# Performance work log

Measured on AMD Instinct MI355X. Metric: run time of the kernel, lower is better.

## Reference

```python
import jax, jax.numpy as jnp
import numpy as np

S, B, D, H = 1024, 64, 512, 512


def setup_inputs() -> dict:
    key = jax.random.key(0)
    ks = jax.random.split(key, 9)
    scale_g = 1.0 / np.sqrt(D + H)  # torch Linear default init range
    def lin(k):
        kw, kb = jax.random.split(k)
        W = jax.random.uniform(kw, (H, D + H), jnp.float32, -scale_g, scale_g)
        b = jax.random.uniform(kb, (H,), jnp.float32, -scale_g, scale_g)
        return W, b
    Wf, bf = lin(ks[0])
    Wi, bi = lin(ks[1])
    Wg, bg = lin(ks[2])
    Wo, bo = lin(ks[3])
    inputs = jax.random.normal(ks[4], (S, B, D), jnp.float32)
    return {"inputs": inputs, "Wf": Wf, "bf": bf, "Wi": Wi, "bi": bi,
            "Wg": Wg, "bg": bg, "Wo": Wo, "bo": bo}


def _lstm(inputs, Wf, bf, Wi, bi, Wg, bg, Wo, bo):
    # inputs: (S, B, D). Precompute the input-to-gate GEMMs for all timesteps
    # in one large matmul (same math: Linear(cat([x,h])) = x@Wx.T + h@Wh.T + b).
    Dd = inputs.shape[-1]
    Wx = jnp.concatenate([Wf[:, :Dd], Wi[:, :Dd], Wg[:, :Dd], Wo[:, :Dd]], axis=0)  # (4H, D)
    Wh = jnp.concatenate([Wf[:, Dd:], Wi[:, Dd:], Wg[:, Dd:], Wo[:, Dd:]], axis=0)  # (4H, H)
    b = jnp.concatenate([bf, bi, bg, bo], axis=0)  # (4H,)
    gx = jnp.einsum('sbd,gd->sbg', inputs, Wx) + b  # (S, B, 4H)
    Hh = Wf.shape[0]

    def step(carry, gx_t):
        hx, cx = carry
        gates = gx_t + hx @ Wh.T  # (B, 4H)
        f = jax.nn.sigmoid(gates[:, 0 * Hh:1 * Hh])
        i = jax.nn.sigmoid(gates[:, 1 * Hh:2 * Hh])
        g = jnp.tanh(gates[:, 2 * Hh:3 * Hh])
        o = jax.nn.sigmoid(gates[:, 3 * Hh:4 * Hh])
        cx = f * cx + i * g
        hx = o * jnp.tanh(cx)
        return (hx, cx), hx

    B_ = inputs.shape[1]
    h0 = jnp.zeros((B_, Hh), inputs.dtype)
    c0 = jnp.zeros((B_, Hh), inputs.dtype)
    (hx, cx), outputs = jax.lax.scan(step, (h0, c0), gx)
    return outputs, hx, cx


def reference(inputs, Wf, bf, Wi, bi, Wg, bg, Wo, bo):
    outputs, hx, cx = _lstm(inputs, Wf, bf, Wi, bi, Wg, bg, Wo, bo)
    return outputs, (hx, cx)
```

## Files before the change

### kernel.cpp

```cpp
#include <hip/hip_runtime.h>

typedef __attribute__((ext_vector_type(8))) short short8;
typedef __attribute__((ext_vector_type(4))) float f32x4;
typedef unsigned int u32;
typedef unsigned short u16;

#define SS 1024
#define BB 64
#define DD 512
#define HH 512

#define WS_XB    0x00000000ULL
#define WS_WPX   0x04000000ULL
#define WS_WPH   0x04200000ULL
#define WS_BIAS  0x04400000ULL
#define WS_HB0   0x04402000ULL
#define WS_HB1   0x04422000ULL
#define WS_BAR   0x04442000ULL

__device__ __forceinline__ u16 f2bf(float x) {
  union { float f; u32 u; } v; v.f = x;
  u32 r = v.u + 0x7fffu + ((v.u >> 16) & 1u);
  return (u16)(r >> 16);
}

__device__ __forceinline__ float sigm(float x) {
  return 1.f / (1.f + __expf(-x));
}
__device__ __forceinline__ float tanh_fast(float x) {
  const float e = __expf(-2.f * __builtin_fabsf(x));
  return __builtin_copysignf((1.f - e) / (1.f + e), x);
}

__global__ __launch_bounds__(256) void pack_x(const float* __restrict__ X,
                                              u16* __restrict__ Xb) {
  const size_t i = ((size_t)blockIdx.x * 256 + threadIdx.x) * 4;
  const float4 v = *(const float4*)(X + i);
  uint2 o;
  o.x = (u32)f2bf(v.x) | ((u32)f2bf(v.y) << 16);
  o.y = (u32)f2bf(v.z) | ((u32)f2bf(v.w) << 16);
  *(uint2*)(Xb + i) = o;
}

__global__ __launch_bounds__(128) void pack_w(
    const float* __restrict__ Wf, const float* __restrict__ bf_,
    const float* __restrict__ Wi, const float* __restrict__ bi_,
    const float* __restrict__ Wg, const float* __restrict__ bg_,
    const float* __restrict__ Wo, const float* __restrict__ bo_,
    u16* __restrict__ Wpx, u16* __restrict__ Wph, float* __restrict__ bias) {
  const int c = blockIdx.x;
  const int g = c & 3, u = c >> 2;
  const float* Wsrc = (g == 0 ? Wf : g == 1 ? Wi : g == 2 ? Wg : Wo) + (size_t)u * 1024;
  const int k = threadIdx.x * 4;
  const float4 vx = *(const float4*)(Wsrc + k);
  const float4 vh = *(const float4*)(Wsrc + 512 + k);
  uint2 ox, oh;
  ox.x = (u32)f2bf(vx.x) | ((u32)f2bf(vx.y) << 16);
  ox.y = (u32)f2bf(vx.z) | ((u32)f2bf(vx.w) << 16);
  oh.x = (u32)f2bf(vh.x) | ((u32)f2bf(vh.y) << 16);
  oh.y = (u32)f2bf(vh.z) | ((u32)f2bf(vh.w) << 16);
  *(uint2*)(Wpx + (size_t)c * 512 + k) = ox;
  *(uint2*)(Wph + (size_t)c * 512 + k) = oh;
  if (threadIdx.x == 0)
    bias[c] = (g == 0 ? bf_ : g == 1 ? bi_ : g == 2 ? bg_ : bo_)[u];
}

__global__ __launch_bounds__(256, 1) void lstm_scan(
    const u16* __restrict__ Wph, const u16* __restrict__ Wpx,
    const u16* __restrict__ Xb, const float* __restrict__ bias,
    u16* __restrict__ hb0, u16* __restrict__ hb1,
    float* __restrict__ out, u32* __restrict__ bar) {
  const int w = blockIdx.x;
  const int tid = threadIdx.x;
  const int lane = tid & 63;
  const int wave = tid >> 6;
  const int m0 = w * 16;
  const int kq = (lane >> 4) * 8;
  const int arow = m0 + (lane & 15);
  const int brow = wave * 16 + (lane & 15);
  const int u_loc = lane >> 4;

  short8 ah[16], ax[16];
#pragma unroll
  for (int kf = 0; kf < 16; ++kf) {
    ah[kf] = *(const short8*)(Wph + (size_t)arow * 512 + kf * 32 + kq);
    ax[kf] = *(const short8*)(Wpx + (size_t)arow * 512 + kf * 32 + kq);
  }
  const float4 b4 = *(const float4*)(bias + m0 + u_loc * 4);
  const f32x4 bias_acc = (f32x4){b4.x, b4.y, b4.z, b4.w};

  short8 bx[16];
#pragma unroll
  for (int kf = 0; kf < 16; ++kf)
    bx[kf] = *(const short8*)(Xb + (size_t)brow * 512 + kf * 32 + kq);
  f32x4 x0 = bias_acc, x1 = (f32x4){0.f, 0.f, 0.f, 0.f}, x2 = x1, x3 = x1;
#pragma unroll
  for (int kf = 0; kf < 16; kf += 4) {
    x0 = __builtin_amdgcn_mfma_f32_16x16x32_bf16(ax[kf + 0], bx[kf + 0], x0, 0, 0, 0);
    x1 = __builtin_amdgcn_mfma_f32_16x16x32_bf16(ax[kf + 1], bx[kf + 1], x1, 0, 0, 0);
    x2 = __builtin_amdgcn_mfma_f32_16x16x32_bf16(ax[kf + 2], bx[kf + 2], x2, 0, 0, 0);
    x3 = __builtin_amdgcn_mfma_f32_16x16x32_bf16(ax[kf + 3], bx[kf + 3], x3, 0, 0, 0);
  }
  f32x4 gxcur = (x0 + x1) + (x2 + x3);
#pragma unroll
  for (int kf = 0; kf < 16; ++kf)
    bx[kf] = *(const short8*)(Xb + ((size_t)64 + brow) * 512 + kf * 32 + kq);

  float c_reg = 0.f;
  __shared__ float ho_lds[64][4];
  __shared__ float co_lds[64][4];

#pragma unroll 1
  for (int t = 0; t < SS; ++t) {
    const u16* hcur = (t & 1) ? hb1 : hb0;
    u16* hnxt = (t & 1) ? hb0 : hb1;

    short8 bh[16];
#pragma unroll
    for (int kf = 0; kf < 16; ++kf)
      bh[kf] = *(const short8*)(hcur + (size_t)brow * 512 + kf * 32 + kq);

    f32x4 ac0 = gxcur;
    f32x4 ac1 = (f32x4){0.f, 0.f, 0.f, 0.f}, ac2 = ac1, ac3 = ac1;
#pragma unroll
    for (int kf = 0; kf < 16; kf += 4) {
      ac0 = __builtin_amdgcn_mfma_f32_16x16x32_bf16(ah[kf + 0], bh[kf + 0], ac0, 0, 0, 0);
      ac1 = __builtin_amdgcn_mfma_f32_16x16x32_bf16(ah[kf + 1], bh[kf + 1], ac1, 0, 0, 0);
      ac2 = __builtin_amdgcn_mfma_f32_16x16x32_bf16(ah[kf + 2], bh[kf + 2], ac2, 0, 0, 0);
      ac3 = __builtin_amdgcn_mfma_f32_16x16x32_bf16(ah[kf + 3], bh[kf + 3], ac3, 0, 0, 0);
    }
    const f32x4 accs = (ac0 + ac1) + (ac2 + ac3);

    const float fs = sigm(accs[0]);
    const float is = sigm(accs[1]);
    const float gv = tanh_fast(accs[2]);
    const float os = sigm(accs[3]);
    c_reg = fs * c_reg + is * gv;
    const float hv = os * tanh_fast(c_reg);

    ho_lds[brow][u_loc] = hv;
    co_lds[brow][u_loc] = c_reg;
    __syncthreads();

    if (tid < 64) {
      const float4 h4 = *(const float4*)(ho_lds[tid]);
      uint2 hb;
      hb.x = (u32)f2bf(h4.x) | ((u32)f2bf(h4.y) << 16);
      hb.y = (u32)f2bf(h4.z) | ((u32)f2bf(h4.w) << 16);
      *(uint2*)(hnxt + (size_t)tid * 512 + w * 4) = hb;
    } else if (tid < 128) {
      const int b = tid - 64;
      const float4 h4 = *(const float4*)(ho_lds[b]);
      *(float4*)(out + (size_t)t * 32768 + (size_t)b * 512 + w * 4) = h4;
      if (t == SS - 1) {
        *(float4*)(out + 33554432 + (size_t)b * 512 + w * 4) = h4;
        const float4 c4 = *(const float4*)(co_lds[b]);
        *(float4*)(out + 33554432 + 32768 + (size_t)b * 512 + w * 4) = c4;
      }
    }

    if (t != SS - 1) {
      if (tid == 0)
        __hip_atomic_fetch_add(bar + (blockIdx.x & 7) * 16, 1u,
                               __ATOMIC_RELEASE, __HIP_MEMORY_SCOPE_AGENT);
      __builtin_amdgcn_sched_barrier(0);

      x0 = bias_acc; x1 = (f32x4){0.f, 0.f, 0.f, 0.f}; x2 = x1; x3 = x1;
#pragma unroll
      for (int kf = 0; kf < 16; kf += 4) {
        x0 = __builtin_amdgcn_mfma_f32_16x16x32_bf16(ax[kf + 0], bx[kf + 0], x0, 0, 0, 0);
        x1 = __builtin_amdgcn_mfma_f32_16x16x32_bf16(ax[kf + 1], bx[kf + 1], x1, 0, 0, 0);
        x2 = __builtin_amdgcn_mfma_f32_16x16x32_bf16(ax[kf + 2], bx[kf + 2], x2, 0, 0, 0);
        x3 = __builtin_amdgcn_mfma_f32_16x16x32_bf16(ax[kf + 3], bx[kf + 3], x3, 0, 0, 0);
      }
      gxcur = (x0 + x1) + (x2 + x3);
      const size_t tnx = (size_t)((t + 2 < SS) ? t + 2 : SS - 1) * 64 + brow;
#pragma unroll
      for (int kf = 0; kf < 16; ++kf)
        bx[kf] = *(const short8*)(Xb + tnx * 512 + kf * 32 + kq);

      const u32 target = (u32)(t + 1) * 16u;
      if (tid < 8) {
        int guard = 0;
#pragma unroll 1
        while (__hip_atomic_load(bar + tid * 16, __ATOMIC_RELAXED,
                                 __HIP_MEMORY_SCOPE_AGENT) < target &&
               ++guard < 8192)
          __builtin_amdgcn_s_sleep(1);
      }
      __syncthreads();
      __builtin_amdgcn_fence(__ATOMIC_ACQUIRE, "agent");
    }
  }
}

extern "C" void kernel_launch(void* const* d_in, const int* in_sizes, int n_in,
                              void* d_out, int out_size, void* d_ws, size_t ws_size,
                              hipStream_t stream) {
  const float* X  = (const float*)d_in[0];
  const float* Wf = (const float*)d_in[1];
  const float* bf_ = (const float*)d_in[2];
  const float* Wi = (const float*)d_in[3];
  const float* bi_ = (const float*)d_in[4];
  const float* Wg = (const float*)d_in[5];
  const float* bg_ = (const float*)d_in[6];
  const float* Wo = (const float*)d_in[7];
  const float* bo_ = (const float*)d_in[8];

  char* ws = (char*)d_ws;
  u16*   Xb   = (u16*)(ws + WS_XB);
  u16*   Wpx  = (u16*)(ws + WS_WPX);
  u16*   Wph  = (u16*)(ws + WS_WPH);
  float* bias = (float*)(ws + WS_BIAS);
  u16*   hb0  = (u16*)(ws + WS_HB0);
  u16*   hb1  = (u16*)(ws + WS_HB1);
  u32*   bar  = (u32*)(ws + WS_BAR);
  float* outp = (float*)d_out;

  hipMemsetAsync(ws + WS_HB0, 0, 0x20000 * 2 + 512, stream);

  pack_x<<<32768, 256, 0, stream>>>(X, Xb);
  pack_w<<<2048, 128, 0, stream>>>(Wf, bf_, Wi, bi_, Wg, bg_, Wo, bo_, Wpx, Wph, bias);

  void* args[] = {(void*)&Wph, (void*)&Wpx, (void*)&Xb, (void*)&bias,
                  (void*)&hb0, (void*)&hb1, (void*)&outp, (void*)&bar};
  hipError_t rc = hipLaunchCooperativeKernel((const void*)lstm_scan,
                                             dim3(128), dim3(256),
                                             args, 0, stream);
  if (rc != hipSuccess) {
    lstm_scan<<<128, 256, 0, stream>>>(Wph, Wpx, Xb, bias, hb0, hb1, outp, bar);
  }
}
```

Before: 13.11 ms.

## Use per-block flag barrier, stage weights in swizzled LDS, nontemporal stores

Replaces the grid barrier, which used atomic increments on eight shared counters, with one release-stored flag per block. A full wave polls all 128 flags and uses a wave-wide vote to decide when to proceed, which is meant to remove atomic contention and cut per-step sync latency. The recurrent and input weight fragments move from registers into XOR-swizzled LDS and are read per MFMA, freeing VGPRs but adding LDS reads to every timestep. The hidden-state and output writes become nontemporal stores.

```diff
diff --git a/kernel.cpp b/kernel.cpp
--- a/kernel.cpp
+++ b/kernel.cpp
@@ -3,6 +3,7 @@
 typedef __attribute__((ext_vector_type(8))) short short8;
 typedef __attribute__((ext_vector_type(4))) float f32x4;
 typedef unsigned int u32;
+typedef unsigned long long u64;
 typedef unsigned short u16;
 
 #define SS 1024
@@ -69,25 +70,45 @@
     const u16* __restrict__ Wph, const u16* __restrict__ Wpx,
     const u16* __restrict__ Xb, const float* __restrict__ bias,
     u16* __restrict__ hb0, u16* __restrict__ hb1,
-    float* __restrict__ out, u32* __restrict__ bar) {
+    float* __restrict__ out, u32* __restrict__ flags) {
   const int w = blockIdx.x;
   const int tid = threadIdx.x;
   const int lane = tid & 63;
   const int wave = tid >> 6;
   const int m0 = w * 16;
   const int kq = (lane >> 4) * 8;
-  const int arow = m0 + (lane & 15);
   const int brow = wave * 16 + (lane & 15);
   const int u_loc = lane >> 4;
 
-  short8 ah[16], ax[16];
-#pragma unroll
-  for (int kf = 0; kf < 16; ++kf) {
-    ah[kf] = *(const short8*)(Wph + (size_t)arow * 512 + kf * 32 + kq);
-    ax[kf] = *(const short8*)(Wpx + (size_t)arow * 512 + kf * 32 + kq);
+  __shared__ u16 ah_lds[8192];
+  __shared__ u16 ax_lds[8192];
+  __shared__ __align__(16) float ho_lds[64][4];
+  __shared__ __align__(16) float co_lds[64][4];
+
+  {
+    const int row = tid >> 4;
+    const int cb  = (tid & 15) * 64;
+    const char* srcH = (const char*)(Wph + (size_t)(m0 + row) * 512);
+    const char* srcX = (const char*)(Wpx + (size_t)(m0 + row) * 512);
+#pragma unroll
+    for (int j = 0; j < 4; ++j) {
+      const int colb = cb + j * 16;
+      const short8 vH = *(const short8*)(srcH + colb);
+      const short8 vX = *(const short8*)(srcX + colb);
+      const int sw = (row * 1024 + colb) ^ ((row & 7) << 4);
+      *(short8*)((char*)ah_lds + sw) = vH;
+      *(short8*)((char*)ax_lds + sw) = vX;
+    }
   }
   const float4 b4 = *(const float4*)(bias + m0 + u_loc * 4);
   const f32x4 bias_acc = (f32x4){b4.x, b4.y, b4.z, b4.w};
+  __syncthreads();
+
+  const int frow = lane & 15;
+  const int fxor = (frow & 7) << 4;
+  const int fbase = frow * 1024 + (lane >> 4) * 16;
+#define LDFRAG(buf, kf) \
+  (*(const short8*)((const char*)(buf) + ((fbase + (kf) * 64) ^ fxor)))
 
   short8 bx[16];
 #pragma unroll
@@ -96,10 +117,10 @@
   f32x4 x0 = bias_acc, x1 = (f32x4){0.f, 0.f, 0.f, 0.f}, x2 = x1, x3 = x1;
 #pragma unroll
   for (int kf = 0; kf < 16; kf += 4) {
-    x0 = __builtin_amdgcn_mfma_f32_16x16x32_bf16(ax[kf + 0], bx[kf + 0], x0, 0, 0, 0);
-    x1 = __builtin_amdgcn_mfma_f32_16x16x32_bf16(ax[kf + 1], bx[kf + 1], x1, 0, 0, 0);
-    x2 = __builtin_amdgcn_mfma_f32_16x16x32_bf16(ax[kf + 2], bx[kf + 2], x2, 0, 0, 0);
-    x3 = __builtin_amdgcn_mfma_f32_16x16x32_bf16(ax[kf + 3], bx[kf + 3], x3, 0, 0, 0);
+    x0 = __builtin_amdgcn_mfma_f32_16x16x32_bf16(LDFRAG(ax_lds, kf + 0), bx[kf + 0], x0, 0, 0, 0);
+    x1 = __builtin_amdgcn_mfma_f32_16x16x32_bf16(LDFRAG(ax_lds, kf + 1), bx[kf + 1], x1, 0, 0, 0);
+    x2 = __builtin_amdgcn_mfma_f32_16x16x32_bf16(LDFRAG(ax_lds, kf + 2), bx[kf + 2], x2, 0, 0, 0);
+    x3 = __builtin_amdgcn_mfma_f32_16x16x32_bf16(LDFRAG(ax_lds, kf + 3), bx[kf + 3], x3, 0, 0, 0);
   }
   f32x4 gxcur = (x0 + x1) + (x2 + x3);
 #pragma unroll
@@ -107,8 +128,6 @@
     bx[kf] = *(const short8*)(Xb + ((size_t)64 + brow) * 512 + kf * 32 + kq);
 
   float c_reg = 0.f;
-  __shared__ float ho_lds[64][4];
-  __shared__ float co_lds[64][4];
 
 #pragma unroll 1
   for (int t = 0; t < SS; ++t) {
@@ -124,10 +143,10 @@
     f32x4 ac1 = (f32x4){0.f, 0.f, 0.f, 0.f}, ac2 = ac1, ac3 = ac1;
 #pragma unroll
     for (int kf = 0; kf < 16; kf += 4) {
-      ac0 = __builtin_amdgcn_mfma_f32_16x16x32_bf16(ah[kf + 0], bh[kf + 0], ac0, 0, 0, 0);
-      ac1 = __builtin_amdgcn_mfma_f32_16x16x32_bf16(ah[kf + 1], bh[kf + 1], ac1, 0, 0, 0);
-      ac2 = __builtin_amdgcn_mfma_f32_16x16x32_bf16(ah[kf + 2], bh[kf + 2], ac2, 0, 0, 0);
-      ac3 = __builtin_amdgcn_mfma_f32_16x16x32_bf16(ah[kf + 3], bh[kf + 3], ac3, 0, 0, 0);
+      ac0 = __builtin_amdgcn_mfma_f32_16x16x32_bf16(LDFRAG(ah_lds, kf + 0), bh[kf + 0], ac0, 0, 0, 0);
+      ac1 = __builtin_amdgcn_mfma_f32_16x16x32_bf16(LDFRAG(ah_lds, kf + 1), bh[kf + 1], ac1, 0, 0, 0);
+      ac2 = __builtin_amdgcn_mfma_f32_16x16x32_bf16(LDFRAG(ah_lds, kf + 2), bh[kf + 2], ac2, 0, 0, 0);
+      ac3 = __builtin_amdgcn_mfma_f32_16x16x32_bf16(LDFRAG(ah_lds, kf + 3), bh[kf + 3], ac3, 0, 0, 0);
     }
     const f32x4 accs = (ac0 + ac1) + (ac2 + ac3);
 
@@ -147,31 +166,35 @@
       uint2 hb;
       hb.x = (u32)f2bf(h4.x) | ((u32)f2bf(h4.y) << 16);
       hb.y = (u32)f2bf(h4.z) | ((u32)f2bf(h4.w) << 16);
-      *(uint2*)(hnxt + (size_t)tid * 512 + w * 4) = hb;
+      __builtin_nontemporal_store(*(const u64*)&hb,
+                                  (u64*)(hnxt + (size_t)tid * 512 + w * 4));
     } else if (tid < 128) {
       const int b = tid - 64;
-      const float4 h4 = *(const float4*)(ho_lds[b]);
-      *(float4*)(out + (size_t)t * 32768 + (size_t)b * 512 + w * 4) = h4;
+      const f32x4 h4 = *(const f32x4*)(ho_lds[b]);
+      __builtin_nontemporal_store(h4,
+          (f32x4*)(out + (size_t)t * 32768 + (size_t)b * 512 + w * 4));
       if (t == SS - 1) {
-        *(float4*)(out + 33554432 + (size_t)b * 512 + w * 4) = h4;
-        const float4 c4 = *(const float4*)(co_lds[b]);
-        *(float4*)(out + 33554432 + 32768 + (size_t)b * 512 + w * 4) = c4;
+        __builtin_nontemporal_store(h4,
+            (f32x4*)(out + 33554432 + (size_t)b * 512 + w * 4));
+        const f32x4 c4 = *(const f32x4*)(co_lds[b]);
+        __builtin_nontemporal_store(c4,
+            (f32x4*)(out + 33554432 + 32768 + (size_t)b * 512 + w * 4));
       }
     }
 
     if (t != SS - 1) {
       if (tid == 0)
-        __hip_atomic_fetch_add(bar + (blockIdx.x & 7) * 16, 1u,
-                               __ATOMIC_RELEASE, __HIP_MEMORY_SCOPE_AGENT);
+        __hip_atomic_store(flags + w, (u32)(t + 1),
+                           __ATOMIC_RELEASE, __HIP_MEMORY_SCOPE_AGENT);
       __builtin_amdgcn_sched_barrier(0);
 
       x0 = bias_acc; x1 = (f32x4){0.f, 0.f, 0.f, 0.f}; x2 = x1; x3 = x1;
 #pragma unroll
       for (int kf = 0; kf < 16; kf += 4) {
-        x0 = __builtin_amdgcn_mfma_f32_16x16x32_bf16(ax[kf + 0], bx[kf + 0], x0, 0, 0, 0);
-        x1 = __builtin_amdgcn_mfma_f32_16x16x32_bf16(ax[kf + 1], bx[kf + 1], x1, 0, 0, 0);
-        x2 = __builtin_amdgcn_mfma_f32_16x16x32_bf16(ax[kf + 2], bx[kf + 2], x2, 0, 0, 0);
-        x3 = __builtin_amdgcn_mfma_f32_16x16x32_bf16(ax[kf + 3], bx[kf + 3], x3, 0, 0, 0);
+        x0 = __builtin_amdgcn_mfma_f32_16x16x32_bf16(LDFRAG(ax_lds, kf + 0), bx[kf + 0], x0, 0, 0, 0);
+        x1 = __builtin_amdgcn_mfma_f32_16x16x32_bf16(LDFRAG(ax_lds, kf + 1), bx[kf + 1], x1, 0, 0, 0);
+        x2 = __builtin_amdgcn_mfma_f32_16x16x32_bf16(LDFRAG(ax_lds, kf + 2), bx[kf + 2], x2, 0, 0, 0);
+        x3 = __builtin_amdgcn_mfma_f32_16x16x32_bf16(LDFRAG(ax_lds, kf + 3), bx[kf + 3], x3, 0, 0, 0);
       }
       gxcur = (x0 + x1) + (x2 + x3);
       const size_t tnx = (size_t)((t + 2 < SS) ? t + 2 : SS - 1) * 64 + brow;
@@ -179,19 +202,23 @@
       for (int kf = 0; kf < 16; ++kf)
         bx[kf] = *(const short8*)(Xb + tnx * 512 + kf * 32 + kq);
 
-      const u32 target = (u32)(t + 1) * 16u;
-      if (tid < 8) {
-        int guard = 0;
+      const u32 target = (u32)(t + 1);
+      if (tid < 64) {
 #pragma unroll 1
-        while (__hip_atomic_load(bar + tid * 16, __ATOMIC_RELAXED,
-                                 __HIP_MEMORY_SCOPE_AGENT) < target &&
-               ++guard < 8192)
+        for (int guard = 0; guard < 8192; ++guard) {
+          const u32 f1 = __hip_atomic_load(flags + tid, __ATOMIC_RELAXED,
+                                           __HIP_MEMORY_SCOPE_AGENT);
+          const u32 f2 = __hip_atomic_load(flags + 64 + tid, __ATOMIC_RELAXED,
+                                           __HIP_MEMORY_SCOPE_AGENT);
+          if (__all((f1 >= target) && (f2 >= target))) break;
           __builtin_amdgcn_s_sleep(1);
+        }
       }
       __syncthreads();
       __builtin_amdgcn_fence(__ATOMIC_ACQUIRE, "agent");
     }
   }
+#undef LDFRAG
 }
 
 extern "C" void kernel_launch(void* const* d_in, const int* in_sizes, int n_in,
@@ -214,7 +241,7 @@
   float* bias = (float*)(ws + WS_BIAS);
   u16*   hb0  = (u16*)(ws + WS_HB0);
   u16*   hb1  = (u16*)(ws + WS_HB1);
-  u32*   bar  = (u32*)(ws + WS_BAR);
+  u32*   flags = (u32*)(ws + WS_BAR);
   float* outp = (float*)d_out;
 
   hipMemsetAsync(ws + WS_HB0, 0, 0x20000 * 2 + 512, stream);
@@ -223,11 +250,11 @@
   pack_w<<<2048, 128, 0, stream>>>(Wf, bf_, Wi, bi_, Wg, bg_, Wo, bo_, Wpx, Wph, bias);
 
   void* args[] = {(void*)&Wph, (void*)&Wpx, (void*)&Xb, (void*)&bias,
-                  (void*)&hb0, (void*)&hb1, (void*)&outp, (void*)&bar};
+                  (void*)&hb0, (void*)&hb1, (void*)&outp, (void*)&flags};
   hipError_t rc = hipLaunchCooperativeKernel((const void*)lstm_scan,
                                              dim3(128), dim3(256),
                                              args, 0, stream);
   if (rc != hipSuccess) {
-    lstm_scan<<<128, 256, 0, stream>>>(Wph, Wpx, Xb, bias, hb0, hb1, outp, bar);
-  }
-}
+    lstm_scan<<<128, 256, 0, stream>>>(Wph, Wpx, Xb, bias, hb0, hb1, outp, flags);
+  }
+}
```

After: 14.17 ms. 1.08x slower.
